# Performance work log

Measured on AMD Instinct MI355X. Metric: run time of the kernel, lower is better.

## Reference

```python
import jax, jax.numpy as jnp
import numpy as np

F = 32        # num_fields
V = 1000      # per-field vocab (field_dims[i])
D = 64        # embed_dim
B = 8192      # batch
P = F * (F - 1) // 2   # 496 pairs
IN = F * D + P          # 2544 MLP input dim
H1, H2, OUT = 1024, 512, 1000


def setup_inputs() -> dict:
    key = jax.random.key(0)
    ks = jax.random.split(key, 8)
    x = jax.random.randint(ks[0], (B, F), 0, V)
    emb_tables = jax.random.normal(ks[1], (F, V, D), dtype=jnp.float32) * 0.05
    W1 = jax.random.normal(ks[2], (IN, H1), dtype=jnp.float32) * (1.0 / np.sqrt(IN))
    b1 = jnp.zeros((H1,), dtype=jnp.float32)
    W2 = jax.random.normal(ks[3], (H1, H2), dtype=jnp.float32) * (1.0 / np.sqrt(H1))
    b2 = jnp.zeros((H2,), dtype=jnp.float32)
    W3 = jax.random.normal(ks[4], (H2, OUT), dtype=jnp.float32) * (1.0 / np.sqrt(H2))
    b3 = jnp.zeros((OUT,), dtype=jnp.float32)
    return {"x": x, "emb_tables": emb_tables, "W1": W1, "b1": b1,
            "W2": W2, "b2": b2, "W3": W3, "b3": b3}


def reference(x, emb_tables, W1, b1, W2, b2, W3, b3):
    # Per-field embedding lookup: e[b, f] = emb_tables[f, x[b, f]]  -> (B, F, D)
    e = emb_tables[jnp.arange(F)[None, :], x]
    # All pairwise inner products via one batched gram matrix, then triu gather
    gram = jnp.einsum('bid,bjd->bij', e, e)            # (B, F, F)
    iu, ju = jnp.triu_indices(F, k=1)
    cross = gram[:, iu, ju]                             # (B, P)
    h = jnp.concatenate([e.reshape(B, F * D), cross], axis=1)  # (B, IN)
    # MLP (dropout is identity in eval mode)
    h = jax.nn.relu(h @ W1 + b1)
    h = jax.nn.relu(h @ W2 + b2)
    logits = h @ W3 + b3
    return jax.nn.sigmoid(logits)
```

## Files before the change

### kernel.cpp

```cpp
#include <hip/hip_runtime.h>
#include <hip/hip_bf16.h>
#include <cmath>

#define F_   32
#define V_   1000
#define D_   64
#define B_   8192
#define IN_RAW  2544
#define IN_PAD  2560
#define H1_  1024
#define H2_  512
#define OUT_RAW 1000
#define OUT_PAD 1024

typedef __attribute__((ext_vector_type(4))) float f32x4;
typedef __attribute__((ext_vector_type(8))) __bf16 bf16x8;

typedef const __attribute__((address_space(1))) void* gptr_t;
typedef __attribute__((address_space(3))) void* lptr_t;

__device__ __forceinline__ void gload_lds16(const void* g, void* l) {
  __builtin_amdgcn_global_load_lds((gptr_t)g, (lptr_t)l, 16, 0, 0);
}

__global__ __launch_bounds__(256)
void interact_kernel(const int* __restrict__ x, const float* __restrict__ emb,
                     __hip_bfloat16* __restrict__ h)
{
  __shared__ __align__(16) __hip_bfloat16 e4[4][32 * 64];
  const int wid  = threadIdx.x >> 6;
  const int lane = threadIdx.x & 63;
  const int b = blockIdx.x * 4 + wid;
  const int* xb = x + b * F_;
  const size_t hrow = (size_t)b * IN_PAD;

#pragma unroll
  for (int it = 0; it < 8; ++it) {
    const int r = it * 4 + (lane >> 4);
    const int d = (lane & 15) * 4;
    const int idx = xb[r];
    const float4 v = *reinterpret_cast<const float4*>(
        &emb[((size_t)r * V_ + idx) * D_ + d]);
    __hip_bfloat16 t[4];
    t[0] = __float2bfloat16(v.x); t[1] = __float2bfloat16(v.y);
    t[2] = __float2bfloat16(v.z); t[3] = __float2bfloat16(v.w);
    const ushort4 pk = *reinterpret_cast<const ushort4*>(t);
    *reinterpret_cast<ushort4*>(&h[hrow + r * 64 + d]) = pk;
    const int ch = (d >> 3) ^ (r & 7);
    *reinterpret_cast<ushort4*>(&e4[wid][r * 64 + ch * 8 + (d & 7)]) = pk;
  }
  __syncthreads();

  f32x4 g[2][2] = {};
#pragma unroll
  for (int kk = 0; kk < 2; ++kk) {
    bf16x8 fa[2];
#pragma unroll
    for (int t = 0; t < 2; ++t) {
      const int r = t * 16 + (lane & 15);
      const int ch = (kk * 4 + (lane >> 4)) ^ (r & 7);
      fa[t] = *reinterpret_cast<const bf16x8*>(&e4[wid][r * 64 + ch * 8]);
    }
#pragma unroll
    for (int ti = 0; ti < 2; ++ti)
#pragma unroll
      for (int tj = 0; tj < 2; ++tj)
        g[ti][tj] = __builtin_amdgcn_mfma_f32_16x16x32_bf16(fa[ti], fa[tj], g[ti][tj], 0, 0, 0);
  }

#pragma unroll
  for (int ti = 0; ti < 2; ++ti)
#pragma unroll
    for (int tj = 0; tj < 2; ++tj) {
      const int jj = tj * 16 + (lane & 15);
#pragma unroll
      for (int q = 0; q < 4; ++q) {
        const int i = ti * 16 + (lane >> 4) * 4 + q;
        if (i < jj) {
          const int p = i * 31 - (i * (i - 1)) / 2 + (jj - i - 1);
          h[hrow + 2048 + p] = __float2bfloat16(g[ti][tj][q]);
        }
      }
    }
  if (lane < IN_PAD - IN_RAW) h[hrow + IN_RAW + lane] = __float2bfloat16(0.f);
}

__global__ __launch_bounds__(256)
void convert_transpose(const float* __restrict__ W, __hip_bfloat16* __restrict__ Wt,
                       int K, int N, int Kpad, int Npad)
{
  __shared__ float t[32][33];
  const int k0 = blockIdx.x * 32, n0 = blockIdx.y * 32;
  const int tx = threadIdx.x, ty = threadIdx.y;
#pragma unroll
  for (int i = 0; i < 4; ++i) {
    int r = ty + i * 8;
    int k = k0 + r, n = n0 + tx;
    t[r][tx] = (k < K && n < N) ? W[(size_t)k * N + n] : 0.f;
  }
  __syncthreads();
#pragma unroll
  for (int i = 0; i < 4; ++i) {
    int r = ty + i * 8;
    Wt[(size_t)(n0 + r) * Kpad + (k0 + tx)] = __float2bfloat16(t[tx][r]);
  }
}

template <int EPI>
__global__ __launch_bounds__(256)
void gemm_bt(const __hip_bfloat16* __restrict__ A,
             const __hip_bfloat16* __restrict__ Bt,
             const float* __restrict__ bias,
             void* __restrict__ Cout,
             int M, int N, int K, int Nreal)
{
  __shared__ __align__(16) __hip_bfloat16 lds[2][2][128 * 64];

  const int tid  = threadIdx.x;
  const int wid  = tid >> 6;
  const int lane = tid & 63;
  const int wr = wid >> 1, wc = wid & 1;
  const int lr = lane & 15;
  const int lhi = lane >> 4;
  const long rowBase = (long)blockIdx.x * 128;
  const long colBase = (long)blockIdx.y * 128;

  f32x4 acc[4][4] = {};

  const int srow = tid >> 3;
  const long scol = (long)(((tid & 7) ^ (srow & 7)) * 8);
  const long aBase = (rowBase + srow) * (long)K + scol;
  const long bBase = (colBase + srow) * (long)K + scol;

  const int NT = K >> 6;

  auto STAGE = [&](int buf, int t) {
    const long k0 = (long)t * 64;
    char* la = (char*)&lds[buf][0][0] + wid * 1024;
    char* lb = (char*)&lds[buf][1][0] + wid * 1024;
#pragma unroll
    for (int j = 0; j < 4; ++j) {
      gload_lds16(A  + aBase + (long)j * 32 * K + k0, la + j * 4096);
      gload_lds16(Bt + bBase + (long)j * 32 * K + k0, lb + j * 4096);
    }
  };

  STAGE(0, 0);
  __syncthreads();

  int cur = 0;
  for (int t = 0; t < NT; ++t) {
    if (t + 1 < NT) STAGE(cur ^ 1, t + 1);

    const __hip_bfloat16* la = &lds[cur][0][0];
    const __hip_bfloat16* lb = &lds[cur][1][0];
#pragma unroll
    for (int kk = 0; kk < 2; ++kk) {
      const int ch = ((kk * 4 + lhi) ^ (lane & 7)) * 8;
      bf16x8 af[4], bfv[4];
#pragma unroll
      for (int m = 0; m < 4; ++m)
        af[m] = *reinterpret_cast<const bf16x8*>(&la[(wr * 64 + m * 16 + lr) * 64 + ch]);
#pragma unroll
      for (int n = 0; n < 4; ++n)
        bfv[n] = *reinterpret_cast<const bf16x8*>(&lb[(wc * 64 + n * 16 + lr) * 64 + ch]);
#pragma unroll
      for (int m = 0; m < 4; ++m)
#pragma unroll
        for (int n = 0; n < 4; ++n)
          acc[m][n] = __builtin_amdgcn_mfma_f32_16x16x32_bf16(af[m], bfv[n], acc[m][n], 0, 0, 0);
    }
    __syncthreads();
    cur ^= 1;
  }

#pragma unroll
  for (int m = 0; m < 4; ++m) {
    const long row0 = rowBase + wr * 64 + m * 16 + lhi * 4;
#pragma unroll
    for (int n = 0; n < 4; ++n) {
      const int col = (int)colBase + wc * 64 + n * 16 + lr;
      const float bv = (col < Nreal) ? bias[col] : 0.f;
#pragma unroll
      for (int j = 0; j < 4; ++j) {
        float v = acc[m][n][j] + bv;
        const long row = row0 + j;
        if (EPI == 0) {
          v = fmaxf(v, 0.f);
          ((__hip_bfloat16*)Cout)[row * N + col] = __float2bfloat16(v);
        } else {
          if (col < Nreal)
            ((float*)Cout)[row * Nreal + col] = 1.f / (1.f + expf(-v));
        }
      }
    }
  }
}

extern "C" void kernel_launch(void* const* d_in, const int* in_sizes, int n_in,
                              void* d_out, int out_size, void* d_ws, size_t ws_size,
                              hipStream_t stream)
{
  const int*   x   = (const int*)  d_in[0];
  const float* emb = (const float*)d_in[1];
  const float* W1  = (const float*)d_in[2];
  const float* b1  = (const float*)d_in[3];
  const float* W2  = (const float*)d_in[4];
  const float* b2  = (const float*)d_in[5];
  const float* W3  = (const float*)d_in[6];
  const float* b3  = (const float*)d_in[7];
  float* out = (float*)d_out;

  char* ws = (char*)d_ws;
  size_t off = 0;
  auto alloc = [&](size_t bytes) { size_t o = off; off = (off + bytes + 255) & ~255ULL; return o; };
  __hip_bfloat16* h   = (__hip_bfloat16*)(ws + alloc((size_t)B_ * IN_PAD * 2));
  __hip_bfloat16* w1t = (__hip_bfloat16*)(ws + alloc((size_t)H1_ * IN_PAD * 2));
  __hip_bfloat16* w2t = (__hip_bfloat16*)(ws + alloc((size_t)H2_ * H1_ * 2));
  __hip_bfloat16* w3t = (__hip_bfloat16*)(ws + alloc((size_t)OUT_PAD * H2_ * 2));
  __hip_bfloat16* h1  = (__hip_bfloat16*)(ws + alloc((size_t)B_ * H1_ * 2));
  __hip_bfloat16* h2  = (__hip_bfloat16*)(ws + alloc((size_t)B_ * H2_ * 2));

  dim3 tb(32, 8);
  convert_transpose<<<dim3(IN_PAD / 32, H1_ / 32), tb, 0, stream>>>(W1, w1t, IN_RAW, H1_, IN_PAD, H1_);
  convert_transpose<<<dim3(H1_ / 32, H2_ / 32), tb, 0, stream>>>(W2, w2t, H1_, H2_, H1_, H2_);
  convert_transpose<<<dim3(H2_ / 32, OUT_PAD / 32), tb, 0, stream>>>(W3, w3t, H2_, OUT_RAW, H2_, OUT_PAD);

  interact_kernel<<<B_ / 4, 256, 0, stream>>>(x, emb, h);

  gemm_bt<0><<<dim3(B_ / 128, H1_ / 128), 256, 0, stream>>>(h, w1t, b1, h1, B_, H1_, IN_PAD, H1_);
  gemm_bt<0><<<dim3(B_ / 128, H2_ / 128), 256, 0, stream>>>(h1, w2t, b2, h2, B_, H2_, H1_, H2_);
  gemm_bt<1><<<dim3(B_ / 128, OUT_PAD / 128), 256, 0, stream>>>(h2, w3t, b3, out, B_, OUT_PAD, H2_, OUT_RAW);
}
```

Before: 192.2 us.

## Merge prep kernels and deepen GEMM pipeline to four-stage K=32 ring

Folds the three weight convert-transpose launches and the embedding/interaction kernel into one prep kernel dispatched by block index, removing launch gaps. The GEMM now stages K=32 tiles into a four-buffer LDS ring with three tiles in flight, using explicit vmcnt waits and raw barriers instead of a double-buffered K=64 loop. The aim is to hide global latency better. In exchange it uses 128KB LDS per block, which caps occupancy at one block per CU, and the new swizzle must stay correct.

```diff
diff --git a/kernel.cpp b/kernel.cpp
--- a/kernel.cpp
+++ b/kernel.cpp
@@ -23,98 +23,110 @@
   __builtin_amdgcn_global_load_lds((gptr_t)g, (lptr_t)l, 16, 0, 0);
 }
 
-__global__ __launch_bounds__(256)
-void interact_kernel(const int* __restrict__ x, const float* __restrict__ emb,
-                     __hip_bfloat16* __restrict__ h)
+#define MF(a, b, c) __builtin_amdgcn_mfma_f32_16x16x32_bf16((a), (b), (c), 0, 0, 0)
+#define SBAR asm volatile("s_barrier" ::: "memory")
+#define WAITV(n) asm volatile("s_waitcnt vmcnt(" #n ")" ::: "memory")
+
+__global__ __launch_bounds__(256)
+void prep_kernel(const int* __restrict__ x, const float* __restrict__ emb,
+                 const float* __restrict__ W1, const float* __restrict__ W2,
+                 const float* __restrict__ W3,
+                 __hip_bfloat16* __restrict__ h, __hip_bfloat16* __restrict__ w1t,
+                 __hip_bfloat16* __restrict__ w2t, __hip_bfloat16* __restrict__ w3t)
 {
-  __shared__ __align__(16) __hip_bfloat16 e4[4][32 * 64];
-  const int wid  = threadIdx.x >> 6;
-  const int lane = threadIdx.x & 63;
-  const int b = blockIdx.x * 4 + wid;
-  const int* xb = x + b * F_;
-  const size_t hrow = (size_t)b * IN_PAD;
-
-#pragma unroll
-  for (int it = 0; it < 8; ++it) {
-    const int r = it * 4 + (lane >> 4);
-    const int d = (lane & 15) * 4;
-    const int idx = xb[r];
-    const float4 v = *reinterpret_cast<const float4*>(
-        &emb[((size_t)r * V_ + idx) * D_ + d]);
-    __hip_bfloat16 t[4];
-    t[0] = __float2bfloat16(v.x); t[1] = __float2bfloat16(v.y);
-    t[2] = __float2bfloat16(v.z); t[3] = __float2bfloat16(v.w);
-    const ushort4 pk = *reinterpret_cast<const ushort4*>(t);
-    *reinterpret_cast<ushort4*>(&h[hrow + r * 64 + d]) = pk;
-    const int ch = (d >> 3) ^ (r & 7);
-    *reinterpret_cast<ushort4*>(&e4[wid][r * 64 + ch * 8 + (d & 7)]) = pk;
-  }
-  __syncthreads();
-
-  f32x4 g[2][2] = {};
-#pragma unroll
-  for (int kk = 0; kk < 2; ++kk) {
-    bf16x8 fa[2];
-#pragma unroll
-    for (int t = 0; t < 2; ++t) {
-      const int r = t * 16 + (lane & 15);
-      const int ch = (kk * 4 + (lane >> 4)) ^ (r & 7);
-      fa[t] = *reinterpret_cast<const bf16x8*>(&e4[wid][r * 64 + ch * 8]);
-    }
+  __shared__ __align__(16) char smem[16384];
+  const int bid = blockIdx.x;
+  const int tid = threadIdx.x;
+
+  if (bid < 3584) {
+    const float* W; __hip_bfloat16* Wt; int K, N, Kpad, kb, nb;
+    if (bid < 2560)      { W = W1; Wt = w1t; K = IN_RAW; N = H1_;     Kpad = IN_PAD; kb = bid % 80; nb = bid / 80; }
+    else if (bid < 3072) { int r = bid - 2560; W = W2; Wt = w2t; K = H1_; N = H2_;   Kpad = H1_;   kb = r % 32;  nb = r / 32; }
+    else                 { int r = bid - 3072; W = W3; Wt = w3t; K = H2_; N = OUT_RAW; Kpad = H2_; kb = r % 16;  nb = r / 16; }
+    float (*t)[33] = (float(*)[33])smem;
+    const int k0 = kb * 32, n0 = nb * 32;
+    const int tx = tid & 31, ty = tid >> 5;
+#pragma unroll
+    for (int i = 0; i < 4; ++i) {
+      int r = ty + i * 8;
+      int k = k0 + r, n = n0 + tx;
+      t[r][tx] = (k < K && n < N) ? W[(size_t)k * N + n] : 0.f;
+    }
+    __syncthreads();
+#pragma unroll
+    for (int i = 0; i < 4; ++i) {
+      int r = ty + i * 8;
+      Wt[(size_t)(n0 + r) * Kpad + (k0 + tx)] = __float2bfloat16(t[tx][r]);
+    }
+  } else {
+    __hip_bfloat16 (*e4)[2048] = (__hip_bfloat16(*)[2048])smem;
+    const int wid  = tid >> 6;
+    const int lane = tid & 63;
+    const int b = (bid - 3584) * 4 + wid;
+    const int* xb = x + b * F_;
+    const size_t hrow = (size_t)b * IN_PAD;
+
+#pragma unroll
+    for (int it = 0; it < 8; ++it) {
+      const int r = it * 4 + (lane >> 4);
+      const int d = (lane & 15) * 4;
+      const int idx = xb[r];
+      const float4 v = *reinterpret_cast<const float4*>(
+          &emb[((size_t)r * V_ + idx) * D_ + d]);
+      __hip_bfloat16 tb[4];
+      tb[0] = __float2bfloat16(v.x); tb[1] = __float2bfloat16(v.y);
+      tb[2] = __float2bfloat16(v.z); tb[3] = __float2bfloat16(v.w);
+      const ushort4 pk = *reinterpret_cast<const ushort4*>(tb);
+      *reinterpret_cast<ushort4*>(&h[hrow + r * 64 + d]) = pk;
+      const int ch = (d >> 3) ^ (r & 7);
+      *reinterpret_cast<ushort4*>(&e4[wid][r * 64 + ch * 8 + (d & 7)]) = pk;
+    }
+    __syncthreads();
+
+    f32x4 g[2][2] = {};
+#pragma unroll
+    for (int kk = 0; kk < 2; ++kk) {
+      bf16x8 fa[2];
+#pragma unroll
+      for (int t2 = 0; t2 < 2; ++t2) {
+        const int r = t2 * 16 + (lane & 15);
+        const int ch = (kk * 4 + (lane >> 4)) ^ (r & 7);
+        fa[t2] = *reinterpret_cast<const bf16x8*>(&e4[wid][r * 64 + ch * 8]);
+      }
+#pragma unroll
+      for (int ti = 0; ti < 2; ++ti)
+#pragma unroll
+        for (int tj = 0; tj < 2; ++tj)
+          g[ti][tj] = MF(fa[ti], fa[tj], g[ti][tj]);
+    }
+
 #pragma unroll
     for (int ti = 0; ti < 2; ++ti)
 #pragma unroll
-      for (int tj = 0; tj < 2; ++tj)
-        g[ti][tj] = __builtin_amdgcn_mfma_f32_16x16x32_bf16(fa[ti], fa[tj], g[ti][tj], 0, 0, 0);
-  }
-
-#pragma unroll
-  for (int ti = 0; ti < 2; ++ti)
-#pragma unroll
-    for (int tj = 0; tj < 2; ++tj) {
-      const int jj = tj * 16 + (lane & 15);
-#pragma unroll
-      for (int q = 0; q < 4; ++q) {
-        const int i = ti * 16 + (lane >> 4) * 4 + q;
-        if (i < jj) {
-          const int p = i * 31 - (i * (i - 1)) / 2 + (jj - i - 1);
-          h[hrow + 2048 + p] = __float2bfloat16(g[ti][tj][q]);
+      for (int tj = 0; tj < 2; ++tj) {
+        const int jj = tj * 16 + (lane & 15);
+#pragma unroll
+        for (int q = 0; q < 4; ++q) {
+          const int i = ti * 16 + (lane >> 4) * 4 + q;
+          if (i < jj) {
+            const int p = i * 31 - (i * (i - 1)) / 2 + (jj - i - 1);
+            h[hrow + 2048 + p] = __float2bfloat16(g[ti][tj][q]);
+          }
         }
       }
-    }
-  if (lane < IN_PAD - IN_RAW) h[hrow + IN_RAW + lane] = __float2bfloat16(0.f);
-}
-
-__global__ __launch_bounds__(256)
-void convert_transpose(const float* __restrict__ W, __hip_bfloat16* __restrict__ Wt,
-                       int K, int N, int Kpad, int Npad)
+    if (lane < IN_PAD - IN_RAW) h[hrow + IN_RAW + lane] = __float2bfloat16(0.f);
+  }
+}
+
+template <int EPI>
+__device__ __forceinline__ void gemm_body(
+    const __hip_bfloat16* __restrict__ A,
+    const __hip_bfloat16* __restrict__ Bt,
+    const float* __restrict__ bias,
+    void* __restrict__ Cout,
+    int M, int N, int K, int Nreal)
 {
-  __shared__ float t[32][33];
-  const int k0 = blockIdx.x * 32, n0 = blockIdx.y * 32;
-  const int tx = threadIdx.x, ty = threadIdx.y;
-#pragma unroll
-  for (int i = 0; i < 4; ++i) {
-    int r = ty + i * 8;
-    int k = k0 + r, n = n0 + tx;
-    t[r][tx] = (k < K && n < N) ? W[(size_t)k * N + n] : 0.f;
-  }
-  __syncthreads();
-#pragma unroll
-  for (int i = 0; i < 4; ++i) {
-    int r = ty + i * 8;
-    Wt[(size_t)(n0 + r) * Kpad + (k0 + tx)] = __float2bfloat16(t[tx][r]);
-  }
-}
-
-template <int EPI>
-__global__ __launch_bounds__(256)
-void gemm_bt(const __hip_bfloat16* __restrict__ A,
-             const __hip_bfloat16* __restrict__ Bt,
-             const float* __restrict__ bias,
-             void* __restrict__ Cout,
-             int M, int N, int K, int Nreal)
-{
-  __shared__ __align__(16) __hip_bfloat16 lds[2][2][128 * 64];
+  __shared__ __align__(16) char lds[4][32768];
 
   const int tid  = threadIdx.x;
   const int wid  = tid >> 6;
@@ -127,51 +139,59 @@
 
   f32x4 acc[4][4] = {};
 
-  const int srow = tid >> 3;
-  const long scol = (long)(((tid & 7) ^ (srow & 7)) * 8);
-  const long aBase = (rowBase + srow) * (long)K + scol;
-  const long bBase = (colBase + srow) * (long)K + scol;
-
-  const int NT = K >> 6;
+  const int prow  = tid >> 2;
+  const int pch   = tid & 3;
+  const int s7    = (prow >> 1) & 7;
+  const int lslot = (((prow & 1) << 2) | pch) ^ s7;
+  const int lrow  = ((prow >> 1) << 1) | (lslot >> 2);
+  const int lch8  = (lslot & 3) << 3;
+  const __hip_bfloat16* A0 = A  + (rowBase + lrow) * (long)K + lch8;
+  const __hip_bfloat16* A1 = A  + (rowBase + 64 + lrow) * (long)K + lch8;
+  const __hip_bfloat16* B0 = Bt + (colBase + lrow) * (long)K + lch8;
+  const __hip_bfloat16* B1 = Bt + (colBase + 64 + lrow) * (long)K + lch8;
+  char* const ldsw = &lds[0][0] + wid * 1024;
+
+  const int NT = K >> 5;
 
   auto STAGE = [&](int buf, int t) {
-    const long k0 = (long)t * 64;
-    char* la = (char*)&lds[buf][0][0] + wid * 1024;
-    char* lb = (char*)&lds[buf][1][0] + wid * 1024;
-#pragma unroll
-    for (int j = 0; j < 4; ++j) {
-      gload_lds16(A  + aBase + (long)j * 32 * K + k0, la + j * 4096);
-      gload_lds16(Bt + bBase + (long)j * 32 * K + k0, lb + j * 4096);
-    }
+    const long k0 = (long)t << 5;
+    char* lb = ldsw + buf * 32768;
+    gload_lds16(A0 + k0, lb);
+    gload_lds16(A1 + k0, lb + 4096);
+    gload_lds16(B0 + k0, lb + 16384);
+    gload_lds16(B1 + k0, lb + 20480);
   };
 
-  STAGE(0, 0);
-  __syncthreads();
-
-  int cur = 0;
+  auto loff = [&](int r, int c) -> int {
+    return ((r >> 1) << 7) + (((((r & 1) << 2) | c) ^ ((r >> 1) & 7)) << 4);
+  };
+
+  auto COMPUTE = [&](int buf) {
+    const char* ba = &lds[0][0] + buf * 32768;
+    const char* bb = ba + 16384;
+    bf16x8 af[4], bv[4];
+#pragma unroll
+    for (int m = 0; m < 4; ++m)
+      af[m] = *reinterpret_cast<const bf16x8*>(ba + loff(wr * 64 + m * 16 + lr, lhi));
+#pragma unroll
+    for (int n = 0; n < 4; ++n)
+      bv[n] = *reinterpret_cast<const bf16x8*>(bb + loff(wc * 64 + n * 16 + lr, lhi));
+#pragma unroll
+    for (int m = 0; m < 4; ++m)
+#pragma unroll
+      for (int n = 0; n < 4; ++n)
+        acc[m][n] = MF(af[m], bv[n], acc[m][n]);
+  };
+
+  STAGE(0, 0); STAGE(1, 1); STAGE(2, 2);
+  WAITV(8); SBAR;
+
   for (int t = 0; t < NT; ++t) {
-    if (t + 1 < NT) STAGE(cur ^ 1, t + 1);
-
-    const __hip_bfloat16* la = &lds[cur][0][0];
-    const __hip_bfloat16* lb = &lds[cur][1][0];
-#pragma unroll
-    for (int kk = 0; kk < 2; ++kk) {
-      const int ch = ((kk * 4 + lhi) ^ (lane & 7)) * 8;
-      bf16x8 af[4], bfv[4];
-#pragma unroll
-      for (int m = 0; m < 4; ++m)
-        af[m] = *reinterpret_cast<const bf16x8*>(&la[(wr * 64 + m * 16 + lr) * 64 + ch]);
-#pragma unroll
-      for (int n = 0; n < 4; ++n)
-        bfv[n] = *reinterpret_cast<const bf16x8*>(&lb[(wc * 64 + n * 16 + lr) * 64 + ch]);
-#pragma unroll
-      for (int m = 0; m < 4; ++m)
-#pragma unroll
-        for (int n = 0; n < 4; ++n)
-          acc[m][n] = __builtin_amdgcn_mfma_f32_16x16x32_bf16(af[m], bfv[n], acc[m][n], 0, 0, 0);
-    }
-    __syncthreads();
-    cur ^= 1;
+    if (t + 3 < NT) STAGE((t + 3) & 3, t + 3);
+    COMPUTE(t & 3);
+    if (t + 3 < NT)      { WAITV(8); SBAR; }
+    else if (t + 2 < NT) { WAITV(4); SBAR; }
+    else if (t + 1 < NT) { WAITV(0); SBAR; }
   }
 
 #pragma unroll
@@ -180,14 +200,13 @@
 #pragma unroll
     for (int n = 0; n < 4; ++n) {
       const int col = (int)colBase + wc * 64 + n * 16 + lr;
-      const float bv = (col < Nreal) ? bias[col] : 0.f;
+      const float bvs = (col < Nreal) ? bias[col] : 0.f;
 #pragma unroll
       for (int j = 0; j < 4; ++j) {
-        float v = acc[m][n][j] + bv;
+        float v = acc[m][n][j] + bvs;
         const long row = row0 + j;
         if (EPI == 0) {
-          v = fmaxf(v, 0.f);
-          ((__hip_bfloat16*)Cout)[row * N + col] = __float2bfloat16(v);
+          ((__hip_bfloat16*)Cout)[row * N + col] = __float2bfloat16(fmaxf(v, 0.f));
         } else {
           if (col < Nreal)
             ((float*)Cout)[row * Nreal + col] = 1.f / (1.f + expf(-v));
@@ -195,6 +214,22 @@
       }
     }
   }
+}
+
+__global__ __launch_bounds__(256)
+void gemm_L1(const __hip_bfloat16* A, const __hip_bfloat16* Bt, const float* bias,
+             void* C, int M, int N, int K, int Nreal) {
+  gemm_body<0>(A, Bt, bias, C, M, N, K, Nreal);
+}
+__global__ __launch_bounds__(256)
+void gemm_L2(const __hip_bfloat16* A, const __hip_bfloat16* Bt, const float* bias,
+             void* C, int M, int N, int K, int Nreal) {
+  gemm_body<0>(A, Bt, bias, C, M, N, K, Nreal);
+}
+__global__ __launch_bounds__(256)
+void gemm_L3(const __hip_bfloat16* A, const __hip_bfloat16* Bt, const float* bias,
+             void* C, int M, int N, int K, int Nreal) {
+  gemm_body<1>(A, Bt, bias, C, M, N, K, Nreal);
 }
 
 extern "C" void kernel_launch(void* const* d_in, const int* in_sizes, int n_in,
@@ -221,14 +256,9 @@
   __hip_bfloat16* h1  = (__hip_bfloat16*)(ws + alloc((size_t)B_ * H1_ * 2));
   __hip_bfloat16* h2  = (__hip_bfloat16*)(ws + alloc((size_t)B_ * H2_ * 2));
 
-  dim3 tb(32, 8);
-  convert_transpose<<<dim3(IN_PAD / 32, H1_ / 32), tb, 0, stream>>>(W1, w1t, IN_RAW, H1_, IN_PAD, H1_);
-  convert_transpose<<<dim3(H1_ / 32, H2_ / 32), tb, 0, stream>>>(W2, w2t, H1_, H2_, H1_, H2_);
-  convert_transpose<<<dim3(H2_ / 32, OUT_PAD / 32), tb, 0, stream>>>(W3, w3t, H2_, OUT_RAW, H2_, OUT_PAD);
-
-  interact_kernel<<<B_ / 4, 256, 0, stream>>>(x, emb, h);
-
-  gemm_bt<0><<<dim3(B_ / 128, H1_ / 128), 256, 0, stream>>>(h, w1t, b1, h1, B_, H1_, IN_PAD, H1_);
-  gemm_bt<0><<<dim3(B_ / 128, H2_ / 128), 256, 0, stream>>>(h1, w2t, b2, h2, B_, H2_, H1_, H2_);
-  gemm_bt<1><<<dim3(B_ / 128, OUT_PAD / 128), 256, 0, stream>>>(h2, w3t, b3, out, B_, OUT_PAD, H2_, OUT_RAW);
-}
+  prep_kernel<<<5632, 256, 0, stream>>>(x, emb, W1, W2, W3, h, w1t, w2t, w3t);
+
+  gemm_L1<<<dim3(B_ / 128, H1_ / 128), 256, 0, stream>>>(h, w1t, b1, h1, B_, H1_, IN_PAD, H1_);
+  gemm_L2<<<dim3(B_ / 128, H2_ / 128), 256, 0, stream>>>(h1, w2t, b2, h2, B_, H2_, H1_, H2_);
+  gemm_L3<<<dim3(B_ / 128, OUT_PAD / 128), 256, 0, stream>>>(h2, w3t, b3, out, B_, OUT_PAD, H2_, OUT_RAW);
+}
```

After: 218.1 us. +13.5%, slower.
